# Kernel optimization log

Measured on AMD Instinct MI355X. Metric: run time of the kernel, lower is better.

The kernel has to match this reference:

```python
import jax, jax.numpy as jnp
import numpy as np

B, T, C, H = 8, 2048, 384, 64

def setup_inputs() -> dict:
    key = jax.random.key(0)
    k1, k2, k3, k4 = jax.random.split(key, 4)
    x = jax.random.normal(k1, (B, T, C), dtype=jnp.float32)
    Wq = jax.random.normal(k2, (C, H), dtype=jnp.float32) * (C ** -0.5)
    Wk = jax.random.normal(k3, (C, H), dtype=jnp.float32) * (C ** -0.5)
    Wv = jax.random.normal(k4, (C, H), dtype=jnp.float32) * (C ** -0.5)
    return {"x": x, "Wq": Wq, "Wk": Wk, "Wv": Wv}

def reference(x, Wq, Wk, Wv):
    # x: (B, T, C); projections: (B, T, H)
    Bn, Tn, Cn = x.shape
    q = jnp.einsum('btc,ch->bth', x, Wq)
    k = jnp.einsum('btc,ch->bth', x, Wk)
    v = jnp.einsum('btc,ch->bth', x, Wv)
    # NOTE: source scales by C**-0.5 (embedding dim), not head_size**-0.5
    weights = jnp.einsum('bth,bsh->bts', q, k) * (Cn ** -0.5)  # (B, T, T)
    causal = jnp.tril(jnp.ones((Tn, Tn), dtype=bool))
    weights = jnp.where(causal, weights, -jnp.inf)
    # NOTE: source applies softmax over dim=1 (query/row axis), reproduced faithfully
    weights = jax.nn.softmax(weights, axis=1)
    # dropout omitted (eval-mode reference)
    return jnp.einsum('bts,bsh->bth', weights, v)
```

## Files before the change

### kernel.cpp

```cpp
#include <hip/hip_runtime.h>
#include <hip/hip_bf16.h>
#include <math.h>

#define Bn 8
#define Tn 2048
#define Cn 384
#define Hn 64
#define SCALE 0.051031036307982884f

using bf16x8 = __attribute__((ext_vector_type(8))) short;
using f32x4  = __attribute__((ext_vector_type(4))) float;

#define MFMA(a, b, c) __builtin_amdgcn_mfma_f32_16x16x32_bf16((a), (b), (c), 0, 0, 0)

static __device__ __forceinline__ short f2bf(float f) {
  unsigned u = __float_as_uint(f);
  u += 0x7fffu + ((u >> 16) & 1u);
  return (short)(u >> 16);
}

__global__ __launch_bounds__(256) void wconv_kernel(
    const float* __restrict__ Wq, const float* __restrict__ Wk,
    const float* __restrict__ Wv, short* __restrict__ WbT) {
  int idx = blockIdx.x * 256 + threadIdx.x;
  int n = idx / 384, k = idx - n * 384;
  const float* W = (n < 64) ? Wq : (n < 128) ? Wk : Wv;
  WbT[idx] = f2bf(W[k * 64 + (n & 63)]);
}

__global__ __launch_bounds__(256) void proj_kernel(
    const float* __restrict__ x, const short* __restrict__ WbT,
    short* __restrict__ qb, short* __restrict__ kb, short* __restrict__ vT) {
  __shared__ short xs[16][392];
  __shared__ short vtile[64][20];
  const int tid = threadIdx.x;
  const int t0 = blockIdx.x * 16;
  const float* xb = x + (size_t)t0 * Cn;
  #pragma unroll
  for (int i = 0; i < 6; ++i) {
    int j = tid + i * 256;
    int row = j / 96, colv = (j - row * 96) * 4;
    float4 v = *(const float4*)(xb + row * Cn + colv);
    short4 s4; s4.x = f2bf(v.x); s4.y = f2bf(v.y); s4.z = f2bf(v.z); s4.w = f2bf(v.w);
    *(short4*)(&xs[row][colv]) = s4;
  }
  __syncthreads();
  const int w = tid >> 6, l15 = tid & 15, quad = (tid & 63) >> 4;
  f32x4 acc[3] = {};
  for (int ks = 0; ks < 12; ++ks) {
    bf16x8 a = *(const bf16x8*)(&xs[l15][ks * 32 + quad * 8]);
    #pragma unroll
    for (int cf = 0; cf < 3; ++cf) {
      bf16x8 bfr = *(const bf16x8*)(WbT + (size_t)(48 * w + 16 * cf + l15) * Cn + ks * 32 + quad * 8);
      acc[cf] = MFMA(a, bfr, acc[cf]);
    }
  }
  #pragma unroll
  for (int cf = 0; cf < 3; ++cf) {
    int cbase = 48 * w + 16 * cf, c = cbase + l15;
    #pragma unroll
    for (int r = 0; r < 4; ++r) {
      int row = t0 + quad * 4 + r;
      short val = f2bf(acc[cf][r]);
      if (cbase < 64)       qb[(size_t)row * Hn + c] = val;
      else if (cbase < 128) kb[(size_t)row * Hn + (c - 64)] = val;
      else                  vtile[c - 128][quad * 4 + r] = val;
    }
  }
  __syncthreads();
  const int b = t0 >> 11, t0l = t0 & 2047;
  int h = tid >> 2, tseg = (tid & 3) * 4;
  *(short4*)(vT + ((size_t)(b * Hn + h)) * Tn + t0l + tseg) =
      *(const short4*)(&vtile[h][tseg]);
}

__global__ __launch_bounds__(256) void colstats_kernel(
    const short* __restrict__ qb, const short* __restrict__ kb,
    float* __restrict__ pL) {
  const int unit = blockIdx.x;
  const int b = unit >> 7, rem = unit & 127;
  const int i = rem >> 2, g = rem & 3;
  const int s0 = i << 6;
  const int q = 32 - i;
  const int klo = (g * q) >> 2, khi = ((g + 1) * q) >> 2;
  const int tid = threadIdx.x, w = tid >> 6, l15 = tid & 15, quad = (tid & 63) >> 4;
  __shared__ float redl[64][17];
  bf16x8 bk[8];
  #pragma unroll
  for (int nf = 0; nf < 4; ++nf) {
    const size_t krow = (size_t)(b * Tn + s0 + 16 * nf + l15) * Hn;
    bk[2 * nf]     = *(const bf16x8*)(kb + krow + quad * 8);
    bk[2 * nf + 1] = *(const bf16x8*)(kb + krow + 32 + quad * 8);
  }
  float l[4] = {0.f, 0.f, 0.f, 0.f};
  const size_t qbase = (size_t)(b * Tn) * Hn;
  auto cload = [&](bf16x8& A0, bf16x8& A1, int k) {
    size_t ar = qbase + (size_t)(s0 + (k << 6) + 16 * w + l15) * Hn;
    A0 = *(const bf16x8*)(qb + ar + quad * 8);
    A1 = *(const bf16x8*)(qb + ar + 32 + quad * 8);
  };
  auto ccomp = [&](bf16x8 A0, bf16x8 A1, int k) {
    f32x4 sc[4] = {};
    #pragma unroll
    for (int nf = 0; nf < 4; ++nf) {
      sc[nf] = MFMA(A0, bk[2 * nf], sc[nf]);
      sc[nf] = MFMA(A1, bk[2 * nf + 1], sc[nf]);
    }
    const bool diag = (k == 0);
    const int tb = s0 + (k << 6) + 16 * w + quad * 4;
    #pragma unroll
    for (int nf = 0; nf < 4; ++nf) {
      int s = s0 + 16 * nf + l15;
      #pragma unroll
      for (int r = 0; r < 4; ++r) {
        float v = sc[nf][r] * SCALE;
        if (diag && (tb + r) < s) v = -INFINITY;
        l[nf] += __expf(v);
      }
    }
  };
  if (klo < khi) {
    bf16x8 a0A, a1A, a0B, a1B;
    cload(a0A, a1A, klo);
    int k = klo;
    while (k + 1 < khi) {
      cload(a0B, a1B, k + 1);
      ccomp(a0A, a1A, k);
      if (k + 2 < khi) cload(a0A, a1A, k + 2);
      ccomp(a0B, a1B, k + 1);
      k += 2;
    }
    if (k < khi) ccomp(a0A, a1A, k);
  }
  #pragma unroll
  for (int nf = 0; nf < 4; ++nf) redl[16 * nf + l15][w * 4 + quad] = l[nf];
  __syncthreads();
  if (tid < 64) {
    float ls = 0.f;
    #pragma unroll
    for (int j = 0; j < 16; ++j) ls += redl[tid][j];
    pL[unit * 64 + tid] = ls;
  }
}

__global__ __launch_bounds__(256) void comb_kernel(
    const float* __restrict__ pL, float* __restrict__ lL) {
  int gid = blockIdx.x * 256 + threadIdx.x;
  int b = gid >> 11, s = gid & 2047, i = s >> 6, cc = s & 63;
  int base = ((b << 5) + i) << 2;
  float L = 0.f;
  #pragma unroll
  for (int g2 = 0; g2 < 4; ++g2) L += pL[(base + g2) * 64 + cc];
  lL[gid] = 1.0f / L;
}

__global__ __launch_bounds__(256) void outp_kernel(
    const short* __restrict__ qb, const short* __restrict__ kb,
    const short* __restrict__ vT, const float* __restrict__ lL,
    float* __restrict__ pOut) {
  const int unit = blockIdx.x;
  const int b = unit >> 7, rem = unit & 127;
  const int tile = 31 - (rem >> 2), g = rem & 3;
  const int nch = tile + 1;
  const int lo = (g * nch) >> 2, hi = ((g + 1) * nch) >> 2;
  if (lo >= hi) return;
  const int t0 = tile << 6;
  const int tid = threadIdx.x, w = tid >> 6, l15 = tid & 15, quad = (tid & 63) >> 4;
  __shared__ short P[4][16][72];
  const int tr = t0 + 16 * w;
  const size_t qrow = (size_t)(b * Tn + tr + l15) * Hn;
  bf16x8 aq0 = *(const bf16x8*)(qb + qrow + quad * 8);
  bf16x8 aq1 = *(const bf16x8*)(qb + qrow + 32 + quad * 8);
  f32x4 acc[4] = {};
  bf16x8 kA[8], vA[8], kB[8], vB[8];
  float rlA[4], rlB[4];
  auto load = [&](bf16x8 (&kk)[8], bf16x8 (&vv)[8], float (&rl)[4], int ch) {
    const int s0 = ch << 6;
    #pragma unroll
    for (int nf = 0; nf < 4; ++nf) {
      const size_t krow = (size_t)(b * Tn + s0 + 16 * nf + l15) * Hn;
      kk[2 * nf]     = *(const bf16x8*)(kb + krow + quad * 8);
      kk[2 * nf + 1] = *(const bf16x8*)(kb + krow + 32 + quad * 8);
      const size_t vrow = (size_t)(b * Hn + 16 * nf + l15) * Tn + s0;
      vv[2 * nf]     = *(const bf16x8*)(vT + vrow + quad * 8);
      vv[2 * nf + 1] = *(const bf16x8*)(vT + vrow + 32 + quad * 8);
      rl[nf] = lL[b * Tn + s0 + 16 * nf + l15];
    }
  };
  auto comp = [&](bf16x8 (&kk)[8], bf16x8 (&vv)[8], float (&rl)[4], int ch) {
    f32x4 sc[4] = {};
    #pragma unroll
    for (int nf = 0; nf < 4; ++nf) {
      sc[nf] = MFMA(aq0, kk[2 * nf], sc[nf]);
      sc[nf] = MFMA(aq1, kk[2 * nf + 1], sc[nf]);
    }
    const int s0 = ch << 6;
    const bool diagc = (ch == tile);
    #pragma unroll
    for (int nf = 0; nf < 4; ++nf) {
      int s = s0 + 16 * nf + l15;
      #pragma unroll
      for (int r = 0; r < 4; ++r) {
        float wgt = __expf(sc[nf][r] * SCALE) * rl[nf];
        if (diagc && s > tr + quad * 4 + r) wgt = 0.f;
        P[w][quad * 4 + r][16 * nf + l15] = f2bf(wgt);
      }
    }
    bf16x8 ap0 = *(const bf16x8*)(&P[w][l15][quad * 8]);
    bf16x8 ap1 = *(const bf16x8*)(&P[w][l15][32 + quad * 8]);
    #pragma unroll
    for (int nf = 0; nf < 4; ++nf) {
      acc[nf] = MFMA(ap0, vv[2 * nf], acc[nf]);
      acc[nf] = MFMA(ap1, vv[2 * nf + 1], acc[nf]);
    }
  };
  load(kA, vA, rlA, lo);
  int ch = lo;
  while (ch + 1 < hi) {
    load(kB, vB, rlB, ch + 1);
    comp(kA, vA, rlA, ch);
    if (ch + 2 < hi) load(kA, vA, rlA, ch + 2);
    comp(kB, vB, rlB, ch + 1);
    ch += 2;
  }
  if (ch < hi) comp(kA, vA, rlA, ch);
  float* dst = pOut + (size_t)g * ((size_t)Bn * Tn * Hn);
  #pragma unroll
  for (int nf = 0; nf < 4; ++nf)
    #pragma unroll
    for (int r = 0; r < 4; ++r)
      dst[(size_t)(b * Tn + tr + quad * 4 + r) * Hn + 16 * nf + l15] = acc[nf][r];
}

__global__ __launch_bounds__(256) void comb2_kernel(
    const float* __restrict__ pOut, float* __restrict__ out) {
  const size_t NN = (size_t)Bn * Tn * Hn;
  size_t idx = ((size_t)blockIdx.x * 256 + threadIdx.x) * 4;
  float4 a = *(const float4*)(pOut + idx);
  float4 b4 = *(const float4*)(pOut + NN + idx);
  float4 c = *(const float4*)(pOut + 2 * NN + idx);
  float4 d = *(const float4*)(pOut + 3 * NN + idx);
  float4 r;
  r.x = a.x + b4.x + c.x + d.x;
  r.y = a.y + b4.y + c.y + d.y;
  r.z = a.z + b4.z + c.z + d.z;
  r.w = a.w + b4.w + c.w + d.w;
  *(float4*)(out + idx) = r;
}

extern "C" void kernel_launch(void* const* d_in, const int* in_sizes, int n_in,
                              void* d_out, int out_size, void* d_ws, size_t ws_size,
                              hipStream_t stream) {
  const float* x  = (const float*)d_in[0];
  const float* Wq = (const float*)d_in[1];
  const float* Wk = (const float*)d_in[2];
  const float* Wv = (const float*)d_in[3];
  char* ws = (char*)d_ws;
  short* qb   = (short*)(ws);
  short* kb   = (short*)(ws + 2097152);
  short* vT   = (short*)(ws + 4194304);
  short* WbT  = (short*)(ws + 6291456);
  float* lL   = (float*)(ws + 6438912);
  float* pL   = (float*)(ws + 6504448);
  float* pOut = (float*)(ws + 8388608);
  float* outp = (float*)d_out;

  hipLaunchKernelGGL(wconv_kernel, dim3(288), dim3(256), 0, stream, Wq, Wk, Wv, WbT);
  hipLaunchKernelGGL(proj_kernel, dim3(Bn * Tn / 16), dim3(256), 0, stream, x, WbT, qb, kb, vT);
  hipLaunchKernelGGL(colstats_kernel, dim3(Bn * 32 * 4), dim3(256), 0, stream, qb, kb, pL);
  hipLaunchKernelGGL(comb_kernel, dim3(64), dim3(256), 0, stream, pL, lL);
  hipLaunchKernelGGL(outp_kernel, dim3(Bn * 32 * 4), dim3(256), 0, stream, qb, kb, vT, lL, pOut);
  hipLaunchKernelGGL(comb2_kernel, dim3(1024), dim3(256), 0, stream, pOut, outp);
}
```

Measured before the change: 158.7 us.

## Pair triangular tiles for balanced split-K and accumulate partials with atomics

The colstats and output kernels now pair tile j with tile 31-j so every block gets an equal 33-chunk span, split into 8 pieces per pair. The old scheme split each tile into 4 uneven pieces, which left work imbalanced across blocks. Partial results are now accumulated with float atomicAdd into L and directly into the output, so the pL/pOut scratch buffers and the comb2 reduction pass are gone. In exchange it needs two memsets, has atomic contention on output rows, and makes floating-point summation order nondeterministic.

New measurement: 156.8 us. About the same (-1.1%).

```diff
diff --git a/kernel.cpp b/kernel.cpp
--- a/kernel.cpp
+++ b/kernel.cpp
@@ -76,176 +76,163 @@
 
 __global__ __launch_bounds__(256) void colstats_kernel(
     const short* __restrict__ qb, const short* __restrict__ kb,
-    float* __restrict__ pL) {
+    float* __restrict__ L) {
   const int unit = blockIdx.x;
   const int b = unit >> 7, rem = unit & 127;
-  const int i = rem >> 2, g = rem & 3;
-  const int s0 = i << 6;
-  const int q = 32 - i;
-  const int klo = (g * q) >> 2, khi = ((g + 1) * q) >> 2;
+  const int j = rem >> 3, u = rem & 7;
+  const int lo = (u * 33) >> 3, hi = ((u + 1) * 33) >> 3;
+  const int big = 32 - j;
   const int tid = threadIdx.x, w = tid >> 6, l15 = tid & 15, quad = (tid & 63) >> 4;
   __shared__ float redl[64][17];
-  bf16x8 bk[8];
-  #pragma unroll
-  for (int nf = 0; nf < 4; ++nf) {
-    const size_t krow = (size_t)(b * Tn + s0 + 16 * nf + l15) * Hn;
-    bk[2 * nf]     = *(const bf16x8*)(kb + krow + quad * 8);
-    bk[2 * nf + 1] = *(const bf16x8*)(kb + krow + 32 + quad * 8);
-  }
-  float l[4] = {0.f, 0.f, 0.f, 0.f};
-  const size_t qbase = (size_t)(b * Tn) * Hn;
-  auto cload = [&](bf16x8& A0, bf16x8& A1, int k) {
-    size_t ar = qbase + (size_t)(s0 + (k << 6) + 16 * w + l15) * Hn;
-    A0 = *(const bf16x8*)(qb + ar + quad * 8);
-    A1 = *(const bf16x8*)(qb + ar + 32 + quad * 8);
-  };
-  auto ccomp = [&](bf16x8 A0, bf16x8 A1, int k) {
-    f32x4 sc[4] = {};
+
+  auto run = [&](const int i, const int k0, const int k1) {
+    if (k0 >= k1) return;
+    const int s0 = i << 6;
+    bf16x8 bk[8];
     #pragma unroll
     for (int nf = 0; nf < 4; ++nf) {
-      sc[nf] = MFMA(A0, bk[2 * nf], sc[nf]);
-      sc[nf] = MFMA(A1, bk[2 * nf + 1], sc[nf]);
-    }
-    const bool diag = (k == 0);
-    const int tb = s0 + (k << 6) + 16 * w + quad * 4;
-    #pragma unroll
-    for (int nf = 0; nf < 4; ++nf) {
-      int s = s0 + 16 * nf + l15;
-      #pragma unroll
-      for (int r = 0; r < 4; ++r) {
-        float v = sc[nf][r] * SCALE;
-        if (diag && (tb + r) < s) v = -INFINITY;
-        l[nf] += __expf(v);
-      }
-    }
-  };
-  if (klo < khi) {
+      const size_t krow = (size_t)(b * Tn + s0 + 16 * nf + l15) * Hn;
+      bk[2 * nf]     = *(const bf16x8*)(kb + krow + quad * 8);
+      bk[2 * nf + 1] = *(const bf16x8*)(kb + krow + 32 + quad * 8);
+    }
+    float l[4] = {0.f, 0.f, 0.f, 0.f};
+    auto cload = [&](bf16x8& A0, bf16x8& A1, int k) {
+      size_t ar = (size_t)(b * Tn + ((i + k) << 6) + 16 * w + l15) * Hn;
+      A0 = *(const bf16x8*)(qb + ar + quad * 8);
+      A1 = *(const bf16x8*)(qb + ar + 32 + quad * 8);
+    };
+    auto ccomp = [&](bf16x8 A0, bf16x8 A1, int k) {
+      f32x4 sc[4] = {};
+      #pragma unroll
+      for (int nf = 0; nf < 4; ++nf) {
+        sc[nf] = MFMA(A0, bk[2 * nf], sc[nf]);
+        sc[nf] = MFMA(A1, bk[2 * nf + 1], sc[nf]);
+      }
+      const bool diag = (k == 0);
+      const int tb = ((i + k) << 6) + 16 * w + quad * 4;
+      #pragma unroll
+      for (int nf = 0; nf < 4; ++nf) {
+        int s = s0 + 16 * nf + l15;
+        #pragma unroll
+        for (int r = 0; r < 4; ++r) {
+          float v = sc[nf][r] * SCALE;
+          if (diag && (tb + r) < s) v = -INFINITY;
+          l[nf] += __expf(v);
+        }
+      }
+    };
     bf16x8 a0A, a1A, a0B, a1B;
-    cload(a0A, a1A, klo);
-    int k = klo;
-    while (k + 1 < khi) {
+    cload(a0A, a1A, k0);
+    int k = k0;
+    while (k + 1 < k1) {
       cload(a0B, a1B, k + 1);
       ccomp(a0A, a1A, k);
-      if (k + 2 < khi) cload(a0A, a1A, k + 2);
+      if (k + 2 < k1) cload(a0A, a1A, k + 2);
       ccomp(a0B, a1B, k + 1);
       k += 2;
     }
-    if (k < khi) ccomp(a0A, a1A, k);
-  }
-  #pragma unroll
-  for (int nf = 0; nf < 4; ++nf) redl[16 * nf + l15][w * 4 + quad] = l[nf];
-  __syncthreads();
-  if (tid < 64) {
-    float ls = 0.f;
-    #pragma unroll
-    for (int j = 0; j < 16; ++j) ls += redl[tid][j];
-    pL[unit * 64 + tid] = ls;
-  }
-}
-
-__global__ __launch_bounds__(256) void comb_kernel(
-    const float* __restrict__ pL, float* __restrict__ lL) {
+    if (k < k1) ccomp(a0A, a1A, k);
+    __syncthreads();
+    #pragma unroll
+    for (int nf = 0; nf < 4; ++nf) redl[16 * nf + l15][w * 4 + quad] = l[nf];
+    __syncthreads();
+    if (tid < 64) {
+      float ls = 0.f;
+      #pragma unroll
+      for (int q2 = 0; q2 < 16; ++q2) ls += redl[tid][q2];
+      atomicAdd(&L[b * Tn + s0 + tid], ls);
+    }
+  };
+  run(j, lo, min(hi, big));
+  run(31 - j, max(lo, big) - big, hi - big);
+}
+
+__global__ __launch_bounds__(256) void inv_kernel(
+    const float* __restrict__ L, float* __restrict__ lL) {
   int gid = blockIdx.x * 256 + threadIdx.x;
-  int b = gid >> 11, s = gid & 2047, i = s >> 6, cc = s & 63;
-  int base = ((b << 5) + i) << 2;
-  float L = 0.f;
-  #pragma unroll
-  for (int g2 = 0; g2 < 4; ++g2) L += pL[(base + g2) * 64 + cc];
-  lL[gid] = 1.0f / L;
+  lL[gid] = 1.0f / L[gid];
 }
 
 __global__ __launch_bounds__(256) void outp_kernel(
     const short* __restrict__ qb, const short* __restrict__ kb,
     const short* __restrict__ vT, const float* __restrict__ lL,
-    float* __restrict__ pOut) {
+    float* __restrict__ out) {
   const int unit = blockIdx.x;
   const int b = unit >> 7, rem = unit & 127;
-  const int tile = 31 - (rem >> 2), g = rem & 3;
-  const int nch = tile + 1;
-  const int lo = (g * nch) >> 2, hi = ((g + 1) * nch) >> 2;
-  if (lo >= hi) return;
-  const int t0 = tile << 6;
+  const int j = rem >> 3, u = rem & 7;
+  const int lo = (u * 33) >> 3, hi = ((u + 1) * 33) >> 3;
+  const int big = 32 - j;
   const int tid = threadIdx.x, w = tid >> 6, l15 = tid & 15, quad = (tid & 63) >> 4;
   __shared__ short P[4][16][72];
-  const int tr = t0 + 16 * w;
-  const size_t qrow = (size_t)(b * Tn + tr + l15) * Hn;
-  bf16x8 aq0 = *(const bf16x8*)(qb + qrow + quad * 8);
-  bf16x8 aq1 = *(const bf16x8*)(qb + qrow + 32 + quad * 8);
-  f32x4 acc[4] = {};
-  bf16x8 kA[8], vA[8], kB[8], vB[8];
-  float rlA[4], rlB[4];
-  auto load = [&](bf16x8 (&kk)[8], bf16x8 (&vv)[8], float (&rl)[4], int ch) {
-    const int s0 = ch << 6;
-    #pragma unroll
-    for (int nf = 0; nf < 4; ++nf) {
-      const size_t krow = (size_t)(b * Tn + s0 + 16 * nf + l15) * Hn;
-      kk[2 * nf]     = *(const bf16x8*)(kb + krow + quad * 8);
-      kk[2 * nf + 1] = *(const bf16x8*)(kb + krow + 32 + quad * 8);
-      const size_t vrow = (size_t)(b * Hn + 16 * nf + l15) * Tn + s0;
-      vv[2 * nf]     = *(const bf16x8*)(vT + vrow + quad * 8);
-      vv[2 * nf + 1] = *(const bf16x8*)(vT + vrow + 32 + quad * 8);
-      rl[nf] = lL[b * Tn + s0 + 16 * nf + l15];
-    }
+
+  auto run = [&](const int tile, const int k0, const int k1) {
+    if (k0 >= k1) return;
+    const int tr = (tile << 6) + 16 * w;
+    const size_t qrow = (size_t)(b * Tn + tr + l15) * Hn;
+    bf16x8 aq0 = *(const bf16x8*)(qb + qrow + quad * 8);
+    bf16x8 aq1 = *(const bf16x8*)(qb + qrow + 32 + quad * 8);
+    f32x4 acc[4] = {};
+    bf16x8 kA[8], vA[8], kB[8], vB[8];
+    float rlA[4], rlB[4];
+    auto load = [&](bf16x8 (&kk)[8], bf16x8 (&vv)[8], float (&rl)[4], int ch) {
+      const int s0 = ch << 6;
+      #pragma unroll
+      for (int nf = 0; nf < 4; ++nf) {
+        const size_t krow = (size_t)(b * Tn + s0 + 16 * nf + l15) * Hn;
+        kk[2 * nf]     = *(const bf16x8*)(kb + krow + quad * 8);
+        kk[2 * nf + 1] = *(const bf16x8*)(kb + krow + 32 + quad * 8);
+        const size_t vrow = (size_t)(b * Hn + 16 * nf + l15) * Tn + s0;
+        vv[2 * nf]     = *(const bf16x8*)(vT + vrow + quad * 8);
+        vv[2 * nf + 1] = *(const bf16x8*)(vT + vrow + 32 + quad * 8);
+        rl[nf] = lL[b * Tn + s0 + 16 * nf + l15];
+      }
+    };
+    auto comp = [&](bf16x8 (&kk)[8], bf16x8 (&vv)[8], float (&rl)[4], int ch) {
+      f32x4 sc[4] = {};
+      #pragma unroll
+      for (int nf = 0; nf < 4; ++nf) {
+        sc[nf] = MFMA(aq0, kk[2 * nf], sc[nf]);
+        sc[nf] = MFMA(aq1, kk[2 * nf + 1], sc[nf]);
+      }
+      const int s0 = ch << 6;
+      const bool diagc = (ch == tile);
+      #pragma unroll
+      for (int nf = 0; nf < 4; ++nf) {
+        int s = s0 + 16 * nf + l15;
+        #pragma unroll
+        for (int r = 0; r < 4; ++r) {
+          float wgt = __expf(sc[nf][r] * SCALE) * rl[nf];
+          if (diagc && s > tr + quad * 4 + r) wgt = 0.f;
+          P[w][quad * 4 + r][16 * nf + l15] = f2bf(wgt);
+        }
+      }
+      bf16x8 ap0 = *(const bf16x8*)(&P[w][l15][quad * 8]);
+      bf16x8 ap1 = *(const bf16x8*)(&P[w][l15][32 + quad * 8]);
+      #pragma unroll
+      for (int nf = 0; nf < 4; ++nf) {
+        acc[nf] = MFMA(ap0, vv[2 * nf], acc[nf]);
+        acc[nf] = MFMA(ap1, vv[2 * nf + 1], acc[nf]);
+      }
+    };
+    load(kA, vA, rlA, k0);
+    int ch = k0;
+    while (ch + 1 < k1) {
+      load(kB, vB, rlB, ch + 1);
+      comp(kA, vA, rlA, ch);
+      if (ch + 2 < k1) load(kA, vA, rlA, ch + 2);
+      comp(kB, vB, rlB, ch + 1);
+      ch += 2;
+    }
+    if (ch < k1) comp(kA, vA, rlA, ch);
+    #pragma unroll
+    for (int nf = 0; nf < 4; ++nf)
+      #pragma unroll
+      for (int r = 0; r < 4; ++r)
+        atomicAdd(&out[(size_t)(b * Tn + tr + quad * 4 + r) * Hn + 16 * nf + l15],
+                  acc[nf][r]);
   };
-  auto comp = [&](bf16x8 (&kk)[8], bf16x8 (&vv)[8], float (&rl)[4], int ch) {
-    f32x4 sc[4] = {};
-    #pragma unroll
-    for (int nf = 0; nf < 4; ++nf) {
-      sc[nf] = MFMA(aq0, kk[2 * nf], sc[nf]);
-      sc[nf] = MFMA(aq1, kk[2 * nf + 1], sc[nf]);
-    }
-    const int s0 = ch << 6;
-    const bool diagc = (ch == tile);
-    #pragma unroll
-    for (int nf = 0; nf < 4; ++nf) {
-      int s = s0 + 16 * nf + l15;
-      #pragma unroll
-      for (int r = 0; r < 4; ++r) {
-        float wgt = __expf(sc[nf][r] * SCALE) * rl[nf];
-        if (diagc && s > tr + quad * 4 + r) wgt = 0.f;
-        P[w][quad * 4 + r][16 * nf + l15] = f2bf(wgt);
-      }
-    }
-    bf16x8 ap0 = *(const bf16x8*)(&P[w][l15][quad * 8]);
-    bf16x8 ap1 = *(const bf16x8*)(&P[w][l15][32 + quad * 8]);
-    #pragma unroll
-    for (int nf = 0; nf < 4; ++nf) {
-      acc[nf] = MFMA(ap0, vv[2 * nf], acc[nf]);
-      acc[nf] = MFMA(ap1, vv[2 * nf + 1], acc[nf]);
-    }
-  };
-  load(kA, vA, rlA, lo);
-  int ch = lo;
-  while (ch + 1 < hi) {
-    load(kB, vB, rlB, ch + 1);
-    comp(kA, vA, rlA, ch);
-    if (ch + 2 < hi) load(kA, vA, rlA, ch + 2);
-    comp(kB, vB, rlB, ch + 1);
-    ch += 2;
-  }
-  if (ch < hi) comp(kA, vA, rlA, ch);
-  float* dst = pOut + (size_t)g * ((size_t)Bn * Tn * Hn);
-  #pragma unroll
-  for (int nf = 0; nf < 4; ++nf)
-    #pragma unroll
-    for (int r = 0; r < 4; ++r)
-      dst[(size_t)(b * Tn + tr + quad * 4 + r) * Hn + 16 * nf + l15] = acc[nf][r];
-}
-
-__global__ __launch_bounds__(256) void comb2_kernel(
-    const float* __restrict__ pOut, float* __restrict__ out) {
-  const size_t NN = (size_t)Bn * Tn * Hn;
-  size_t idx = ((size_t)blockIdx.x * 256 + threadIdx.x) * 4;
-  float4 a = *(const float4*)(pOut + idx);
-  float4 b4 = *(const float4*)(pOut + NN + idx);
-  float4 c = *(const float4*)(pOut + 2 * NN + idx);
-  float4 d = *(const float4*)(pOut + 3 * NN + idx);
-  float4 r;
-  r.x = a.x + b4.x + c.x + d.x;
-  r.y = a.y + b4.y + c.y + d.y;
-  r.z = a.z + b4.z + c.z + d.z;
-  r.w = a.w + b4.w + c.w + d.w;
-  *(float4*)(out + idx) = r;
+  run(31 - j, lo, min(hi, big));
+  run(j, max(lo, big) - big, hi - big);
 }
 
 extern "C" void kernel_launch(void* const* d_in, const int* in_sizes, int n_in,
@@ -260,15 +247,15 @@
   short* kb   = (short*)(ws + 2097152);
   short* vT   = (short*)(ws + 4194304);
   short* WbT  = (short*)(ws + 6291456);
-  float* lL   = (float*)(ws + 6438912);
-  float* pL   = (float*)(ws + 6504448);
-  float* pOut = (float*)(ws + 8388608);
+  float* L    = (float*)(ws + 6438912);
+  float* lL   = (float*)(ws + 6504448);
   float* outp = (float*)d_out;
 
+  hipMemsetAsync(L, 0, (size_t)Bn * Tn * 4, stream);
+  hipMemsetAsync(outp, 0, (size_t)Bn * Tn * Hn * 4, stream);
   hipLaunchKernelGGL(wconv_kernel, dim3(288), dim3(256), 0, stream, Wq, Wk, Wv, WbT);
   hipLaunchKernelGGL(proj_kernel, dim3(Bn * Tn / 16), dim3(256), 0, stream, x, WbT, qb, kb, vT);
-  hipLaunchKernelGGL(colstats_kernel, dim3(Bn * 32 * 4), dim3(256), 0, stream, qb, kb, pL);
-  hipLaunchKernelGGL(comb_kernel, dim3(64), dim3(256), 0, stream, pL, lL);
-  hipLaunchKernelGGL(outp_kernel, dim3(Bn * 32 * 4), dim3(256), 0, stream, qb, kb, vT, lL, pOut);
-  hipLaunchKernelGGL(comb2_kernel, dim3(1024), dim3(256), 0, stream, pOut, outp);
-}
+  hipLaunchKernelGGL(colstats_kernel, dim3(1024), dim3(256), 0, stream, qb, kb, L);
+  hipLaunchKernelGGL(inv_kernel, dim3(64), dim3(256), 0, stream, L, lL);
+  hipLaunchKernelGGL(outp_kernel, dim3(1024), dim3(256), 0, stream, qb, kb, vT, lL, outp);
+}
```
